# Optimization experiments

Measured on AMD Instinct MI355X. Metric: run time of the kernel, lower is better.

## Reference

```python
import jax, jax.numpy as jnp
import numpy as np

EMB = 16
N_LEFT = 200000
N_RIGHT = 200000
N_EDGES = 4000000


def _linear_params(key, out_dim, in_dim, bias=True):
    k1, k2 = jax.random.split(key)
    bound = 1.0 / np.sqrt(in_dim)
    W = jax.random.uniform(k1, (out_dim, in_dim), minval=-bound, maxval=bound, dtype=jnp.float32)
    if bias:
        b = jax.random.uniform(k2, (out_dim,), minval=-bound, maxval=bound, dtype=jnp.float32)
        return W, b
    return W


def setup_inputs() -> dict:
    key = jax.random.key(0)
    ks = jax.random.split(key, 12)
    left_features = jax.random.normal(ks[0], (N_LEFT, EMB), dtype=jnp.float32)
    right_features = jax.random.normal(ks[1], (N_RIGHT, EMB), dtype=jnp.float32)
    edge_features = jax.random.normal(ks[2], (N_EDGES, 1), dtype=jnp.float32)
    left_idx = jax.random.randint(ks[3], (N_EDGES,), 0, N_LEFT)
    right_idx = jax.random.randint(ks[4], (N_EDGES,), 0, N_RIGHT)
    edge_indices = jnp.stack([left_idx, right_idx], axis=0).astype(jnp.int64)

    W_left, b_left = _linear_params(ks[5], EMB, EMB, bias=True)
    W_edge = _linear_params(ks[6], EMB, 1, bias=False)
    W_right = _linear_params(ks[7], EMB, EMB, bias=False)
    W_final, b_final = _linear_params(ks[8], EMB, EMB, bias=True)
    W_post, b_post = _linear_params(ks[9], EMB, EMB, bias=True)
    W_out1, b_out1 = _linear_params(ks[10], EMB, 2 * EMB, bias=True)
    W_out2, b_out2 = _linear_params(ks[11], EMB, EMB, bias=True)

    return {
        "left_features": left_features,
        "edge_features": edge_features,
        "right_features": right_features,
        "edge_indices": edge_indices,
        "W_left": W_left, "b_left": b_left,
        "W_edge": W_edge,
        "W_right": W_right,
        "W_final": W_final, "b_final": b_final,
        "W_post": W_post, "b_post": b_post,
        "W_out1": W_out1, "b_out1": b_out1,
        "W_out2": W_out2, "b_out2": b_out2,
    }


def reference(left_features, edge_features, right_features, edge_indices,
              W_left, b_left, W_edge, W_right, W_final, b_final,
              W_post, b_post, W_out1, b_out1, W_out2, b_out2):
    n_right = right_features.shape[0]
    left_idx = edge_indices[0]
    right_idx = edge_indices[1]

    # per-edge message: Linear(left gathered) + edge Linear + Linear(right gathered)
    pre = (left_features[left_idx] @ W_left.T + b_left
           + edge_features @ W_edge.T
           + right_features[right_idx] @ W_right.T)  # [E, emb]
    msg = jax.nn.relu(pre) @ W_final.T + b_final     # fm_final: ReLU -> Linear

    # scatter-add aggregate per right node
    aggregated = jax.ops.segment_sum(msg, right_idx, num_segments=n_right)  # [n_right, emb]

    post = jax.nn.relu(aggregated) @ W_post.T + b_post  # post: ReLU -> Linear
    cat = jnp.concatenate([post, right_features], axis=-1)  # [n_right, 2*emb]
    h = jax.nn.relu(cat @ W_out1.T + b_out1)
    return h @ W_out2.T + b_out2
```

## Files before the change

### kernel.cpp

```cpp
#include <hip/hip_runtime.h>
#include <hip/hip_bf16.h>

#define EMB 16
#define EPT 4

typedef _Float16 half8 __attribute__((ext_vector_type(8)));

__global__ __launch_bounds__(256) void node_transform2_kernel(
    const float* __restrict__ left, const float* __restrict__ right,
    const float* __restrict__ Wl, const float* __restrict__ bl,
    const float* __restrict__ Wr,
    _Float16* __restrict__ TL, _Float16* __restrict__ TR, int NL, int NR) {
    __shared__ float sWl[EMB * EMB], sWr[EMB * EMB], sbl[EMB];
    if (threadIdx.x < EMB * EMB) {
        sWl[threadIdx.x] = Wl[threadIdx.x];
        sWr[threadIdx.x] = Wr[threadIdx.x];
    }
    if (threadIdx.x < EMB) sbl[threadIdx.x] = bl[threadIdx.x];
    __syncthreads();

    int n = blockIdx.x * blockDim.x + threadIdx.x;
    if (n >= NL + NR) return;
    bool is_left = (n < NL);
    const float* X = is_left ? (left + (size_t)n * EMB)
                             : (right + (size_t)(n - NL) * EMB);
    _Float16* Y = is_left ? (TL + (size_t)n * EMB)
                          : (TR + (size_t)(n - NL) * EMB);
    const float* sW = is_left ? sWl : sWr;

    float x[EMB];
    const float4* xp = (const float4*)X;
    float4 x0 = xp[0], x1 = xp[1], x2 = xp[2], x3 = xp[3];
    x[0] = x0.x; x[1] = x0.y; x[2] = x0.z; x[3] = x0.w;
    x[4] = x1.x; x[5] = x1.y; x[6] = x1.z; x[7] = x1.w;
    x[8] = x2.x; x[9] = x2.y; x[10] = x2.z; x[11] = x2.w;
    x[12] = x3.x; x[13] = x3.y; x[14] = x3.z; x[15] = x3.w;

    float y[EMB];
#pragma unroll
    for (int j = 0; j < EMB; ++j) {
        float a = is_left ? sbl[j] : 0.0f;
#pragma unroll
        for (int k = 0; k < EMB; ++k) a = fmaf(sW[j * EMB + k], x[k], a);
        y[j] = a;
    }

    half8* yp = (half8*)Y;
    half8 h0, h1;
#pragma unroll
    for (int k = 0; k < 8; ++k) h0[k] = (_Float16)y[k];
#pragma unroll
    for (int k = 0; k < 8; ++k) h1[k] = (_Float16)y[8 + k];
    yp[0] = h0;
    yp[1] = h1;
}

__global__ __launch_bounds__(256) void edge_scatter_kernel(
    const int* __restrict__ idx, const float* __restrict__ ef,
    const _Float16* __restrict__ TL, const _Float16* __restrict__ TR,
    const float* __restrict__ wedge, const float* __restrict__ Wf,
    const float* __restrict__ bf, float* __restrict__ S, int E, int G) {
    int gid = blockIdx.x * blockDim.x + threadIdx.x;
    int g = gid >> 4;
    int t = gid & 15;

    float we = wedge[t];
    float bft = bf[t];
    float wrow[EMB];
    {
        const float4* wp = (const float4*)(Wf + t * EMB);
        float4 w0 = wp[0], w1 = wp[1], w2 = wp[2], w3 = wp[3];
        wrow[0] = w0.x; wrow[1] = w0.y; wrow[2] = w0.z; wrow[3] = w0.w;
        wrow[4] = w1.x; wrow[5] = w1.y; wrow[6] = w1.z; wrow[7] = w1.w;
        wrow[8] = w2.x; wrow[9] = w2.y; wrow[10] = w2.z; wrow[11] = w2.w;
        wrow[12] = w3.x; wrow[13] = w3.y; wrow[14] = w3.z; wrow[15] = w3.w;
    }

    int l[EPT], r[EPT];
    float efv[EPT];
    bool valid[EPT];
#pragma unroll
    for (int j = 0; j < EPT; ++j) {
        int e = g + j * G;
        valid[j] = (e < E);
        int ec = valid[j] ? e : 0;
        l[j] = idx[ec];
        r[j] = idx[E + ec];
        efv[j] = ef[ec];
    }

    _Float16 ah[EPT], bh[EPT];
#pragma unroll
    for (int j = 0; j < EPT; ++j) {
        ah[j] = TL[(size_t)l[j] * EMB + t];
        bh[j] = TR[(size_t)r[j] * EMB + t];
    }

#pragma unroll
    for (int j = 0; j < EPT; ++j) {
        float v = fmaxf((float)ah[j] + (float)bh[j] + efv[j] * we, 0.0f);
        int vi = __float_as_int(v);
        float w = bft;
#define SWIZ_STEP(K)                                                          \
        {                                                                     \
            float vk = __int_as_float(                                        \
                __builtin_amdgcn_ds_swizzle(vi, ((K) << 5) | 0x10));          \
            w = fmaf(wrow[K], vk, w);                                         \
        }
        SWIZ_STEP(0)  SWIZ_STEP(1)  SWIZ_STEP(2)  SWIZ_STEP(3)
        SWIZ_STEP(4)  SWIZ_STEP(5)  SWIZ_STEP(6)  SWIZ_STEP(7)
        SWIZ_STEP(8)  SWIZ_STEP(9)  SWIZ_STEP(10) SWIZ_STEP(11)
        SWIZ_STEP(12) SWIZ_STEP(13) SWIZ_STEP(14) SWIZ_STEP(15)
#undef SWIZ_STEP
        if (valid[j]) atomicAdd(S + (size_t)r[j] * EMB + t, w);
    }
}

__global__ __launch_bounds__(256) void epilogue_kernel(
    const float* __restrict__ S, const float* __restrict__ right,
    const float* __restrict__ Wp, const float* __restrict__ bp,
    const float* __restrict__ Wo1, const float* __restrict__ bo1,
    const float* __restrict__ Wo2, const float* __restrict__ bo2,
    float* __restrict__ out, int N) {
    __shared__ float sWp[256], sWo2[256], sWo1[512];
    __shared__ float sbp[16], sbo1[16], sbo2[16];
    for (int i = threadIdx.x; i < 256; i += blockDim.x) {
        sWp[i] = Wp[i]; sWo2[i] = Wo2[i];
    }
    for (int i = threadIdx.x; i < 512; i += blockDim.x) sWo1[i] = Wo1[i];
    if (threadIdx.x < 16) {
        sbp[threadIdx.x] = bp[threadIdx.x];
        sbo1[threadIdx.x] = bo1[threadIdx.x];
        sbo2[threadIdx.x] = bo2[threadIdx.x];
    }
    __syncthreads();

    int n = blockIdx.x * blockDim.x + threadIdx.x;
    if (n >= N) return;

    float ra[EMB];
    {
        const float4* sp = (const float4*)(S + (size_t)n * EMB);
        float4 a0 = sp[0], a1 = sp[1], a2 = sp[2], a3 = sp[3];
        ra[0] = fmaxf(a0.x, 0.0f); ra[1] = fmaxf(a0.y, 0.0f);
        ra[2] = fmaxf(a0.z, 0.0f); ra[3] = fmaxf(a0.w, 0.0f);
        ra[4] = fmaxf(a1.x, 0.0f); ra[5] = fmaxf(a1.y, 0.0f);
        ra[6] = fmaxf(a1.z, 0.0f); ra[7] = fmaxf(a1.w, 0.0f);
        ra[8] = fmaxf(a2.x, 0.0f); ra[9] = fmaxf(a2.y, 0.0f);
        ra[10] = fmaxf(a2.z, 0.0f); ra[11] = fmaxf(a2.w, 0.0f);
        ra[12] = fmaxf(a3.x, 0.0f); ra[13] = fmaxf(a3.y, 0.0f);
        ra[14] = fmaxf(a3.z, 0.0f); ra[15] = fmaxf(a3.w, 0.0f);
    }

    float p[EMB];
#pragma unroll
    for (int j = 0; j < EMB; ++j) {
        float a = sbp[j];
#pragma unroll
        for (int k = 0; k < EMB; ++k) a = fmaf(sWp[j * EMB + k], ra[k], a);
        p[j] = a;
    }

    float rf[EMB];
    {
        const float4* rp = (const float4*)(right + (size_t)n * EMB);
        float4 a0 = rp[0], a1 = rp[1], a2 = rp[2], a3 = rp[3];
        rf[0] = a0.x; rf[1] = a0.y; rf[2] = a0.z; rf[3] = a0.w;
        rf[4] = a1.x; rf[5] = a1.y; rf[6] = a1.z; rf[7] = a1.w;
        rf[8] = a2.x; rf[9] = a2.y; rf[10] = a2.z; rf[11] = a2.w;
        rf[12] = a3.x; rf[13] = a3.y; rf[14] = a3.z; rf[15] = a3.w;
    }

    float h[EMB];
#pragma unroll
    for (int j = 0; j < EMB; ++j) {
        float a = sbo1[j];
#pragma unroll
        for (int k = 0; k < EMB; ++k) a = fmaf(sWo1[j * 32 + k], p[k], a);
#pragma unroll
        for (int k = 0; k < EMB; ++k) a = fmaf(sWo1[j * 32 + 16 + k], rf[k], a);
        h[j] = fmaxf(a, 0.0f);
    }

    float o[EMB];
#pragma unroll
    for (int j = 0; j < EMB; ++j) {
        float a = sbo2[j];
#pragma unroll
        for (int k = 0; k < EMB; ++k) a = fmaf(sWo2[j * EMB + k], h[k], a);
        o[j] = a;
    }

    float4* op = (float4*)(out + (size_t)n * EMB);
    op[0] = make_float4(o[0], o[1], o[2], o[3]);
    op[1] = make_float4(o[4], o[5], o[6], o[7]);
    op[2] = make_float4(o[8], o[9], o[10], o[11]);
    op[3] = make_float4(o[12], o[13], o[14], o[15]);
}

extern "C" void kernel_launch(void* const* d_in, const int* in_sizes, int n_in,
                              void* d_out, int out_size, void* d_ws, size_t ws_size,
                              hipStream_t stream) {
    const float* left  = (const float*)d_in[0];
    const float* ef    = (const float*)d_in[1];
    const float* right = (const float*)d_in[2];
    const int*   eidx  = (const int*)d_in[3];
    const float* W_left  = (const float*)d_in[4];
    const float* b_left  = (const float*)d_in[5];
    const float* W_edge  = (const float*)d_in[6];
    const float* W_right = (const float*)d_in[7];
    const float* W_final = (const float*)d_in[8];
    const float* b_final = (const float*)d_in[9];
    const float* W_post  = (const float*)d_in[10];
    const float* b_post  = (const float*)d_in[11];
    const float* W_out1  = (const float*)d_in[12];
    const float* b_out1  = (const float*)d_in[13];
    const float* W_out2  = (const float*)d_in[14];
    const float* b_out2  = (const float*)d_in[15];

    const int NL = in_sizes[0] / EMB;
    const int NR = in_sizes[2] / EMB;
    const int E  = in_sizes[1];

    size_t tl_b = (size_t)NL * EMB * 2;
    size_t tr_b = (size_t)NR * EMB * 2;
    char* ws = (char*)d_ws;
    _Float16* TL = (_Float16*)ws;
    _Float16* TR = (_Float16*)(ws + tl_b);
    float* S = (float*)(ws + tl_b + tr_b);

    (void)hipMemsetAsync(S, 0, (size_t)NR * EMB * 4, stream);

    node_transform2_kernel<<<(NL + NR + 255) / 256, 256, 0, stream>>>(
        left, right, W_left, b_left, W_right, TL, TR, NL, NR);

    {
        int G = (E + EPT - 1) / EPT;
        long long threads = (long long)G * 16;
        int blocks = (int)((threads + 255) / 256);
        edge_scatter_kernel<<<blocks, 256, 0, stream>>>(
            eidx, ef, TL, TR, W_edge, W_final, b_final, S, E, G);
    }

    epilogue_kernel<<<(NR + 255) / 256, 256, 0, stream>>>(
        S, right, W_post, b_post, W_out1, b_out1, W_out2, b_out2,
        (float*)d_out, NR);
}
```

Before: 354.9 us.

## Bin edges by destination bucket and aggregate in LDS with linearity hoist

Replaces the global-atomic edge scatter with a two-pass scheme. A binning kernel counting-sorts edges into fixed-capacity buckets of 391 destination rows, packing the left index, local row and edge feature into one payload. A per-bucket kernel then accumulates ReLU(pre) into shared memory with LDS atomics, keeps a per-row edge count, and fuses the epilogue. The W_final linear layer is hoisted past the sum (W_final·Σv + count·b_final), removing the per-edge swizzle matmul. Risks: a fixed CAP of 16384 silently drops edges if a bucket overflows, the payload costs an extra global write and read, and the large LDS footprint limits occupancy.

```diff
diff --git a/kernel.cpp b/kernel.cpp
--- a/kernel.cpp
+++ b/kernel.cpp
@@ -1,8 +1,13 @@
 #include <hip/hip_runtime.h>
 #include <hip/hip_bf16.h>
+#include <hip/hip_fp16.h>
 
 #define EMB 16
+#define RPB 391
+#define MAXNB 512
+#define CAP 16384
 #define EPT 4
+#define NBIN_BLOCKS 512
 
 typedef _Float16 half8 __attribute__((ext_vector_type(8)));
 
@@ -55,147 +60,186 @@
     yp[1] = h1;
 }
 
-__global__ __launch_bounds__(256) void edge_scatter_kernel(
+__global__ __launch_bounds__(256) void binning_kernel(
     const int* __restrict__ idx, const float* __restrict__ ef,
-    const _Float16* __restrict__ TL, const _Float16* __restrict__ TR,
-    const float* __restrict__ wedge, const float* __restrict__ Wf,
-    const float* __restrict__ bf, float* __restrict__ S, int E, int G) {
-    int gid = blockIdx.x * blockDim.x + threadIdx.x;
-    int g = gid >> 4;
-    int t = gid & 15;
-
-    float we = wedge[t];
-    float bft = bf[t];
-    float wrow[EMB];
-    {
-        const float4* wp = (const float4*)(Wf + t * EMB);
-        float4 w0 = wp[0], w1 = wp[1], w2 = wp[2], w3 = wp[3];
-        wrow[0] = w0.x; wrow[1] = w0.y; wrow[2] = w0.z; wrow[3] = w0.w;
-        wrow[4] = w1.x; wrow[5] = w1.y; wrow[6] = w1.z; wrow[7] = w1.w;
-        wrow[8] = w2.x; wrow[9] = w2.y; wrow[10] = w2.z; wrow[11] = w2.w;
-        wrow[12] = w3.x; wrow[13] = w3.y; wrow[14] = w3.z; wrow[15] = w3.w;
-    }
-
-    int l[EPT], r[EPT];
-    float efv[EPT];
-    bool valid[EPT];
-#pragma unroll
-    for (int j = 0; j < EPT; ++j) {
-        int e = g + j * G;
-        valid[j] = (e < E);
-        int ec = valid[j] ? e : 0;
-        l[j] = idx[ec];
-        r[j] = idx[E + ec];
-        efv[j] = ef[ec];
-    }
-
-    _Float16 ah[EPT], bh[EPT];
-#pragma unroll
-    for (int j = 0; j < EPT; ++j) {
-        ah[j] = TL[(size_t)l[j] * EMB + t];
-        bh[j] = TR[(size_t)r[j] * EMB + t];
-    }
-
-#pragma unroll
-    for (int j = 0; j < EPT; ++j) {
-        float v = fmaxf((float)ah[j] + (float)bh[j] + efv[j] * we, 0.0f);
-        int vi = __float_as_int(v);
-        float w = bft;
-#define SWIZ_STEP(K)                                                          \
-        {                                                                     \
-            float vk = __int_as_float(                                        \
-                __builtin_amdgcn_ds_swizzle(vi, ((K) << 5) | 0x10));          \
-            w = fmaf(wrow[K], vk, w);                                         \
-        }
-        SWIZ_STEP(0)  SWIZ_STEP(1)  SWIZ_STEP(2)  SWIZ_STEP(3)
-        SWIZ_STEP(4)  SWIZ_STEP(5)  SWIZ_STEP(6)  SWIZ_STEP(7)
-        SWIZ_STEP(8)  SWIZ_STEP(9)  SWIZ_STEP(10) SWIZ_STEP(11)
-        SWIZ_STEP(12) SWIZ_STEP(13) SWIZ_STEP(14) SWIZ_STEP(15)
-#undef SWIZ_STEP
-        if (valid[j]) atomicAdd(S + (size_t)r[j] * EMB + t, w);
-    }
-}
-
-__global__ __launch_bounds__(256) void epilogue_kernel(
-    const float* __restrict__ S, const float* __restrict__ right,
+    uint2* __restrict__ payload, unsigned int* __restrict__ gcursor,
+    int E, int NB, int per) {
+    __shared__ unsigned int hist[MAXNB];
+    __shared__ unsigned int cur[MAXNB];
+    int tid = threadIdx.x;
+    for (int b = tid; b < NB; b += 256) hist[b] = 0;
+    __syncthreads();
+
+    int start = blockIdx.x * per;
+    int end = min(E, start + per);
+
+    for (int e = start + tid; e < end; e += 256) {
+        int r = idx[E + e];
+        atomicAdd(&hist[r / RPB], 1u);
+    }
+    __syncthreads();
+
+    for (int b = tid; b < NB; b += 256) {
+        unsigned int h = hist[b];
+        cur[b] = h ? atomicAdd(&gcursor[b], h) : 0u;
+    }
+    __syncthreads();
+
+    for (int e = start + tid; e < end; e += 256) {
+        int l = idx[e];
+        int r = idx[E + e];
+        int b = r / RPB;
+        int rlo = r - b * RPB;
+        unsigned int slot = atomicAdd(&cur[b], 1u);
+        if (slot < CAP)
+            payload[(size_t)b * CAP + slot] =
+                make_uint2((unsigned)l | ((unsigned)rlo << 18),
+                           __float_as_uint(ef[e]));
+    }
+}
+
+__global__ __launch_bounds__(256) void bucket_compute_kernel(
+    const uint2* __restrict__ payload, const unsigned int* __restrict__ gcursor,
+    const _Float16* __restrict__ TL, const _Float16* __restrict__ TRg,
+    const float* __restrict__ right, const float* __restrict__ wedge,
+    const float* __restrict__ Wf, const float* __restrict__ bfi,
     const float* __restrict__ Wp, const float* __restrict__ bp,
     const float* __restrict__ Wo1, const float* __restrict__ bo1,
     const float* __restrict__ Wo2, const float* __restrict__ bo2,
-    float* __restrict__ out, int N) {
-    __shared__ float sWp[256], sWo2[256], sWo1[512];
-    __shared__ float sbp[16], sbo1[16], sbo2[16];
-    for (int i = threadIdx.x; i < 256; i += blockDim.x) {
-        sWp[i] = Wp[i]; sWo2[i] = Wo2[i];
-    }
-    for (int i = threadIdx.x; i < 512; i += blockDim.x) sWo1[i] = Wo1[i];
-    if (threadIdx.x < 16) {
-        sbp[threadIdx.x] = bp[threadIdx.x];
-        sbo1[threadIdx.x] = bo1[threadIdx.x];
-        sbo2[threadIdx.x] = bo2[threadIdx.x];
-    }
-    __syncthreads();
-
-    int n = blockIdx.x * blockDim.x + threadIdx.x;
-    if (n >= N) return;
-
-    float ra[EMB];
+    float* __restrict__ out, int NR) {
+    __shared__ _Float16 sTR[RPB * EMB];
+    __shared__ float sS[RPB * EMB];
+    __shared__ float sCnt[RPB];
+    __shared__ float sWf[256], sWp[256], sWo1[512], sWo2[256];
+    __shared__ float sbf[16], sbp[16], sbo1[16], sbo2[16], swe[16];
+
+    int tid = threadIdx.x;
+    int b = blockIdx.x;
+    int row0 = b * RPB;
+    int rows = min(RPB, NR - row0);
+
+    if (tid < 256) { sWf[tid] = Wf[tid]; sWp[tid] = Wp[tid]; sWo2[tid] = Wo2[tid]; }
+    for (int i = tid; i < 512; i += 256) sWo1[i] = Wo1[i];
+    if (tid < 16) {
+        sbf[tid] = bfi[tid]; sbp[tid] = bp[tid];
+        sbo1[tid] = bo1[tid]; sbo2[tid] = bo2[tid];
+        swe[tid] = wedge[tid];
+    }
     {
-        const float4* sp = (const float4*)(S + (size_t)n * EMB);
-        float4 a0 = sp[0], a1 = sp[1], a2 = sp[2], a3 = sp[3];
-        ra[0] = fmaxf(a0.x, 0.0f); ra[1] = fmaxf(a0.y, 0.0f);
-        ra[2] = fmaxf(a0.z, 0.0f); ra[3] = fmaxf(a0.w, 0.0f);
-        ra[4] = fmaxf(a1.x, 0.0f); ra[5] = fmaxf(a1.y, 0.0f);
-        ra[6] = fmaxf(a1.z, 0.0f); ra[7] = fmaxf(a1.w, 0.0f);
-        ra[8] = fmaxf(a2.x, 0.0f); ra[9] = fmaxf(a2.y, 0.0f);
-        ra[10] = fmaxf(a2.z, 0.0f); ra[11] = fmaxf(a2.w, 0.0f);
-        ra[12] = fmaxf(a3.x, 0.0f); ra[13] = fmaxf(a3.y, 0.0f);
-        ra[14] = fmaxf(a3.z, 0.0f); ra[15] = fmaxf(a3.w, 0.0f);
-    }
-
-    float p[EMB];
-#pragma unroll
-    for (int j = 0; j < EMB; ++j) {
-        float a = sbp[j];
-#pragma unroll
-        for (int k = 0; k < EMB; ++k) a = fmaf(sWp[j * EMB + k], ra[k], a);
-        p[j] = a;
-    }
-
-    float rf[EMB];
-    {
-        const float4* rp = (const float4*)(right + (size_t)n * EMB);
-        float4 a0 = rp[0], a1 = rp[1], a2 = rp[2], a3 = rp[3];
-        rf[0] = a0.x; rf[1] = a0.y; rf[2] = a0.z; rf[3] = a0.w;
-        rf[4] = a1.x; rf[5] = a1.y; rf[6] = a1.z; rf[7] = a1.w;
-        rf[8] = a2.x; rf[9] = a2.y; rf[10] = a2.z; rf[11] = a2.w;
-        rf[12] = a3.x; rf[13] = a3.y; rf[14] = a3.z; rf[15] = a3.w;
-    }
-
-    float h[EMB];
-#pragma unroll
-    for (int j = 0; j < EMB; ++j) {
-        float a = sbo1[j];
-#pragma unroll
-        for (int k = 0; k < EMB; ++k) a = fmaf(sWo1[j * 32 + k], p[k], a);
-#pragma unroll
-        for (int k = 0; k < EMB; ++k) a = fmaf(sWo1[j * 32 + 16 + k], rf[k], a);
-        h[j] = fmaxf(a, 0.0f);
-    }
-
-    float o[EMB];
-#pragma unroll
-    for (int j = 0; j < EMB; ++j) {
-        float a = sbo2[j];
-#pragma unroll
-        for (int k = 0; k < EMB; ++k) a = fmaf(sWo2[j * EMB + k], h[k], a);
-        o[j] = a;
-    }
-
-    float4* op = (float4*)(out + (size_t)n * EMB);
-    op[0] = make_float4(o[0], o[1], o[2], o[3]);
-    op[1] = make_float4(o[4], o[5], o[6], o[7]);
-    op[2] = make_float4(o[8], o[9], o[10], o[11]);
-    op[3] = make_float4(o[12], o[13], o[14], o[15]);
+        const unsigned int* src = (const unsigned int*)(TRg + (size_t)row0 * EMB);
+        unsigned int* dst = (unsigned int*)sTR;
+        for (int i = tid; i < rows * 8; i += 256) dst[i] = src[i];
+    }
+    for (int i = tid; i < rows * EMB; i += 256) sS[i] = 0.0f;
+    for (int i = tid; i < rows; i += 256) sCnt[i] = 0.0f;
+    __syncthreads();
+
+    int count = min((int)gcursor[b], CAP);
+    int g = tid >> 4;
+    int t = tid & 15;
+    float we = swe[t];
+    const uint2* pay = payload + (size_t)b * CAP;
+
+    int iters = (count + 16 * EPT - 1) / (16 * EPT);
+    for (int it = 0; it < iters; ++it) {
+        int ebase = it * (16 * EPT) + g;
+        uint2 p[EPT];
+        bool val[EPT];
+#pragma unroll
+        for (int m = 0; m < EPT; ++m) {
+            int e = ebase + m * 16;
+            val[m] = (e < count);
+            p[m] = pay[val[m] ? e : 0];
+        }
+        _Float16 tlv[EPT];
+        int rl[EPT];
+        float efq[EPT];
+#pragma unroll
+        for (int m = 0; m < EPT; ++m) {
+            int l = p[m].x & 0x3FFFF;
+            rl[m] = (int)(p[m].x >> 18);
+            efq[m] = __uint_as_float(p[m].y);
+            tlv[m] = TL[(size_t)l * EMB + t];
+        }
+#pragma unroll
+        for (int m = 0; m < EPT; ++m) {
+            float v = fmaxf((float)tlv[m] + (float)sTR[rl[m] * EMB + t]
+                            + efq[m] * we, 0.0f);
+            if (val[m]) {
+                atomicAdd(&sS[rl[m] * EMB + t], v);
+                if (t == 0) atomicAdd(&sCnt[rl[m]], 1.0f);
+            }
+        }
+    }
+    __syncthreads();
+
+    for (int i = tid; i < rows; i += 256) {
+        int gr = row0 + i;
+        float s[EMB];
+        {
+            const float4* sp = (const float4*)(sS + i * EMB);
+            float4 a0 = sp[0], a1 = sp[1], a2 = sp[2], a3 = sp[3];
+            s[0] = a0.x; s[1] = a0.y; s[2] = a0.z; s[3] = a0.w;
+            s[4] = a1.x; s[5] = a1.y; s[6] = a1.z; s[7] = a1.w;
+            s[8] = a2.x; s[9] = a2.y; s[10] = a2.z; s[11] = a2.w;
+            s[12] = a3.x; s[13] = a3.y; s[14] = a3.z; s[15] = a3.w;
+        }
+        float c = sCnt[i];
+
+        float ra[EMB];
+#pragma unroll
+        for (int j = 0; j < EMB; ++j) {
+            float a = c * sbf[j];
+#pragma unroll
+            for (int k = 0; k < EMB; ++k) a = fmaf(sWf[j * EMB + k], s[k], a);
+            ra[j] = fmaxf(a, 0.0f);
+        }
+
+        float pch[EMB];
+#pragma unroll
+        for (int j = 0; j < EMB; ++j) {
+            float a = sbp[j];
+#pragma unroll
+            for (int k = 0; k < EMB; ++k) a = fmaf(sWp[j * EMB + k], ra[k], a);
+            pch[j] = a;
+        }
+
+        float rf[EMB];
+        {
+            const float4* rp = (const float4*)(right + (size_t)gr * EMB);
+            float4 a0 = rp[0], a1 = rp[1], a2 = rp[2], a3 = rp[3];
+            rf[0] = a0.x; rf[1] = a0.y; rf[2] = a0.z; rf[3] = a0.w;
+            rf[4] = a1.x; rf[5] = a1.y; rf[6] = a1.z; rf[7] = a1.w;
+            rf[8] = a2.x; rf[9] = a2.y; rf[10] = a2.z; rf[11] = a2.w;
+            rf[12] = a3.x; rf[13] = a3.y; rf[14] = a3.z; rf[15] = a3.w;
+        }
+
+        float h[EMB];
+#pragma unroll
+        for (int j = 0; j < EMB; ++j) {
+            float a = sbo1[j];
+#pragma unroll
+            for (int k = 0; k < EMB; ++k) a = fmaf(sWo1[j * 32 + k], pch[k], a);
+#pragma unroll
+            for (int k = 0; k < EMB; ++k) a = fmaf(sWo1[j * 32 + 16 + k], rf[k], a);
+            h[j] = fmaxf(a, 0.0f);
+        }
+
+        float o[EMB];
+#pragma unroll
+        for (int j = 0; j < EMB; ++j) {
+            float a = sbo2[j];
+#pragma unroll
+            for (int k = 0; k < EMB; ++k) a = fmaf(sWo2[j * EMB + k], h[k], a);
+            o[j] = a;
+        }
+
+        float4* op = (float4*)(out + (size_t)gr * EMB);
+        op[0] = make_float4(o[0], o[1], o[2], o[3]);
+        op[1] = make_float4(o[4], o[5], o[6], o[7]);
+        op[2] = make_float4(o[8], o[9], o[10], o[11]);
+        op[3] = make_float4(o[12], o[13], o[14], o[15]);
+    }
 }
 
 extern "C" void kernel_launch(void* const* d_in, const int* in_sizes, int n_in,
@@ -221,28 +265,30 @@
     const int NL = in_sizes[0] / EMB;
     const int NR = in_sizes[2] / EMB;
     const int E  = in_sizes[1];
-
-    size_t tl_b = (size_t)NL * EMB * 2;
-    size_t tr_b = (size_t)NR * EMB * 2;
+    const int NB = (NR + RPB - 1) / RPB;
+
+    size_t tl_b  = (size_t)NL * EMB * 2;
+    size_t tr_b  = (size_t)NR * EMB * 2;
+    size_t pay_b = (size_t)NB * CAP * sizeof(uint2);
     char* ws = (char*)d_ws;
     _Float16* TL = (_Float16*)ws;
     _Float16* TR = (_Float16*)(ws + tl_b);
-    float* S = (float*)(ws + tl_b + tr_b);
-
-    (void)hipMemsetAsync(S, 0, (size_t)NR * EMB * 4, stream);
+    uint2* payload = (uint2*)(ws + tl_b + tr_b);
+    unsigned int* gcursor = (unsigned int*)(ws + tl_b + tr_b + pay_b);
+
+    (void)hipMemsetAsync(gcursor, 0, (size_t)NB * 4, stream);
 
     node_transform2_kernel<<<(NL + NR + 255) / 256, 256, 0, stream>>>(
         left, right, W_left, b_left, W_right, TL, TR, NL, NR);
 
     {
-        int G = (E + EPT - 1) / EPT;
-        long long threads = (long long)G * 16;
-        int blocks = (int)((threads + 255) / 256);
-        edge_scatter_kernel<<<blocks, 256, 0, stream>>>(
-            eidx, ef, TL, TR, W_edge, W_final, b_final, S, E, G);
-    }
-
-    epilogue_kernel<<<(NR + 255) / 256, 256, 0, stream>>>(
-        S, right, W_post, b_post, W_out1, b_out1, W_out2, b_out2,
-        (float*)d_out, NR);
-}
+        int per = (E + NBIN_BLOCKS - 1) / NBIN_BLOCKS;
+        binning_kernel<<<NBIN_BLOCKS, 256, 0, stream>>>(
+            eidx, ef, payload, gcursor, E, NB, per);
+    }
+
+    bucket_compute_kernel<<<NB, 256, 0, stream>>>(
+        payload, gcursor, TL, TR, right, W_edge,
+        W_final, b_final, W_post, b_post,
+        W_out1, b_out1, W_out2, b_out2, (float*)d_out, NR);
+}
```

After: 674.0 us. 89.9% more time.
